# Optimization experiments

Measured on AMD Instinct MI355X. Metric: run time of the kernel, lower is better.

## Reference

```python
import jax, jax.numpy as jnp
import numpy as np

B = 2            # batch size
GRID = 256       # BEV grid H = W
M = 30000        # number of pillars (voxels)
NPTS = 200000    # number of points
IN_C = 16
VOXEL = 0.4      # voxel_size[:2]
PC_MIN = -51.2   # pc_range[:2]
DS = 2           # prod(ds_layer_strides)


def _bn(x, g, b):
    # eval-mode BatchNorm with running_mean=0, running_var=1 (eps absorbed into g)
    return x * g + b


def _conv(x, k, stride):
    # 3x3 conv, padding=1 (spconv SparseConv2d / SubMConv2d with pad k//2), NHWC
    return jax.lax.conv_general_dilated(
        x, k, (stride, stride), ((1, 1), (1, 1)),
        dimension_numbers=('NHWC', 'HWIO', 'NHWC'))


def _active_mask(occ, stride):
    # active output sites of a sparse conv = any active input in the 3x3 receptive field
    pooled = jax.lax.reduce_window(occ, -jnp.inf, jax.lax.max,
                                   (1, 3, 3, 1), (1, stride, stride, 1),
                                   ((0, 0), (1, 1), (1, 1), (0, 0)))
    return (pooled > 0).astype(occ.dtype)


def _forward(features, pfn_w0, pfn_g0, pfn_b0, pfn_w1, pfn_g1, pfn_b1,
             b1_kd, b1_gd, b1_bd, b1_k1, b1_g1, b1_b1, b1_k2, b1_g2, b1_b2,
             b2_kd, b2_gd, b2_bd, b2_k1, b2_g1, b2_b1, b2_k2, b2_g2, b2_b2,
             unq, unq_inv, grid_size):
    # pillar mode: cols 0:2 are xy; convert to (fractional) voxel coordinates
    pos = (features[:, :2] - PC_MIN) / VOXEL  # [N,2] = (px, py)

    # PFN layer 0 (not last): linear(16->16) + BN + ReLU, concat per-pillar max
    h = jax.nn.relu(_bn(features @ pfn_w0, pfn_g0, pfn_b0))            # [N,16]
    hmax = jax.ops.segment_max(h, unq_inv, num_segments=M)             # [M,16]
    h = jnp.concatenate([h, hmax[unq_inv]], axis=1)                    # [N,32]
    # PFN layer 1 (last): linear(32->64) + BN + ReLU
    h = jax.nn.relu(_bn(h @ pfn_w1, pfn_g1, pfn_b1))                   # [N,64]

    # scatter_max pooling points -> pillars
    fv = jax.ops.segment_max(h, unq_inv, num_segments=M)               # [M,64]

    Hn = grid_size
    img = jnp.zeros((B, Hn, Hn, fv.shape[1]), fv.dtype)
    img = img.at[unq[:, 0], unq[:, 1], unq[:, 2]].set(fv)              # dense BEV, NHWC
    occ = jnp.zeros((B, Hn, Hn, 1), fv.dtype)
    occ = occ.at[unq[:, 0], unq[:, 1], unq[:, 2]].set(1.0)

    # block 1: SparseConvBlock(stride=1) + SparseBasicBlock (dense math, masked to active sites)
    occ1 = _active_mask(occ, 1)
    x = jax.nn.relu(_bn(_conv(img, b1_kd, 1), b1_gd, b1_bd)) * occ1
    y = jax.nn.relu(_bn(_conv(x, b1_k1, 1), b1_g1, b1_b1)) * occ1
    y = _bn(_conv(y, b1_k2, 1), b1_g2, b1_b2) * occ1
    x = jax.nn.relu(x + y)

    # block 2: SparseConvBlock(stride=2) + SparseBasicBlock
    occ2 = _active_mask(occ1, 2)
    x = jax.nn.relu(_bn(_conv(x, b2_kd, 2), b2_gd, b2_bd)) * occ2
    y = jax.nn.relu(_bn(_conv(x, b2_k1, 1), b2_g1, b2_b1)) * occ2
    y = _bn(_conv(y, b2_k2, 1), b2_g2, b2_b2) * occ2
    x = jax.nn.relu(x + y)                                             # [B,H/2,W/2,128]

    # bilinear gather at per-point downsampled positions (px -> W axis, py -> H axis)
    bidx = unq[unq_inv, 0]
    px = pos[:, 0] / DS
    py = pos[:, 1] / DS
    Hc, Wc = x.shape[1], x.shape[2]
    x0 = jnp.clip(jnp.floor(px).astype(jnp.int32), 0, Wc - 1)
    x1 = jnp.clip(jnp.floor(px).astype(jnp.int32) + 1, 0, Wc - 1)
    y0 = jnp.clip(jnp.floor(py).astype(jnp.int32), 0, Hc - 1)
    y1 = jnp.clip(jnp.floor(py).astype(jnp.int32) + 1, 0, Hc - 1)
    Ia = x[bidx, y0, x0]
    Ib = x[bidx, y1, x0]
    Ic = x[bidx, y0, x1]
    Id = x[bidx, y1, x1]
    x0f, x1f = x0.astype(px.dtype), x1.astype(px.dtype)
    y0f, y1f = y0.astype(py.dtype), y1.astype(py.dtype)
    wa = ((x1f - px) * (y1f - py))[:, None]
    wb = ((x1f - px) * (py - y0f))[:, None]
    wc = ((px - x0f) * (y1f - py))[:, None]
    wd = ((px - x0f) * (py - y0f))[:, None]
    return Ia * wa + Ib * wb + Ic * wc + Id * wd                       # [N,128]


def setup_inputs() -> dict:
    rng = np.random.default_rng(0)
    d = {}
    d['features'] = jnp.asarray(rng.standard_normal((NPTS, IN_C)).astype(np.float32))
    # unique voxel coords (batch, y, x)
    lin = rng.choice(B * GRID * GRID, size=M, replace=False)
    d['unq'] = jnp.asarray(np.stack([lin // (GRID * GRID), (lin // GRID) % GRID, lin % GRID], 1).astype(np.int32))
    # every pillar gets at least one point
    d['unq_inv'] = jnp.asarray(np.concatenate([np.arange(M), rng.integers(0, M, NPTS - M)]).astype(np.int32))
    d['grid_size'] = GRID

    def w(*s):
        fan = int(np.prod(s[:-1]))
        return jnp.asarray((rng.standard_normal(s) / np.sqrt(fan)).astype(np.float32))

    def g(c):
        return jnp.asarray((0.5 + 0.5 * rng.random(c)).astype(np.float32))

    def bb(c):
        return jnp.asarray((0.1 * rng.standard_normal(c)).astype(np.float32))

    d['pfn_w0'] = w(IN_C, 16); d['pfn_g0'] = g(16); d['pfn_b0'] = bb(16)
    d['pfn_w1'] = w(32, 64);   d['pfn_g1'] = g(64); d['pfn_b1'] = bb(64)
    d['b1_kd'] = w(3, 3, 64, 64);   d['b1_gd'] = g(64);  d['b1_bd'] = bb(64)
    d['b1_k1'] = w(3, 3, 64, 64);   d['b1_g1'] = g(64);  d['b1_b1'] = bb(64)
    d['b1_k2'] = w(3, 3, 64, 64);   d['b1_g2'] = g(64);  d['b1_b2'] = bb(64)
    d['b2_kd'] = w(3, 3, 64, 128);  d['b2_gd'] = g(128); d['b2_bd'] = bb(128)
    d['b2_k1'] = w(3, 3, 128, 128); d['b2_g1'] = g(128); d['b2_b1'] = bb(128)
    d['b2_k2'] = w(3, 3, 128, 128); d['b2_g2'] = g(128); d['b2_b2'] = bb(128)
    return d


def reference(features, unq, unq_inv, grid_size,
              pfn_w0, pfn_g0, pfn_b0, pfn_w1, pfn_g1, pfn_b1,
              b1_kd, b1_gd, b1_bd, b1_k1, b1_g1, b1_b1, b1_k2, b1_g2, b1_b2,
              b2_kd, b2_gd, b2_bd, b2_k1, b2_g1, b2_b1, b2_k2, b2_g2, b2_b2):
    return _forward(features, pfn_w0, pfn_g0, pfn_b0, pfn_w1, pfn_g1, pfn_b1,
                    b1_kd, b1_gd, b1_bd, b1_k1, b1_g1, b1_b1, b1_k2, b1_g2, b1_b2,
                    b2_kd, b2_gd, b2_bd, b2_k1, b2_g1, b2_b1, b2_k2, b2_g2, b2_b2,
                    unq, unq_inv, grid_size)
```

## Files before the change

### kernel.cpp

```cpp
#include <hip/hip_runtime.h>
#include <hip/hip_bf16.h>

#define NPTS    200000
#define MPIL    30000
#define BATCH   2
#define GRID0   256
#define PCMIN   (-51.2f)
#define VOXEL0  (0.4f)
#define NCHUNK  118

#define SLOT_B  ((size_t)16777216)
#define SLOT_F  ((size_t)33554432)

#define W0F 0
#define W1F 256
#define FB1 9216
#define FB2 156672
#define FB3 304128
#define FB4 451584
#define FB5 746496
#define FB6 1336320

#define WS_FLAG 0
#define WS_OCC8 64
#define WS_OCC1 (64 + 131072)
#define WS_OCC2 (64 + 262144)
#define WS_HMAX 393280
#define WS_CNT  2313280
#define WS_OFF  2433280
#define WS_CUR  2553344
#define WS_IDX  2673344
#define WS_LOC  3473344
#define WS_BS   3593344
#define WS_FX   393344

typedef __attribute__((ext_vector_type(8))) short v8s;
typedef __attribute__((ext_vector_type(4))) float f32x4;

static __device__ __forceinline__ float b2f(__hip_bfloat16 v) { return __bfloat162float(v); }
static __device__ __forceinline__ unsigned short f2bbits(float f) {
    __hip_bfloat16 h = __float2bfloat16(f);
    union { __hip_bfloat16 h; unsigned short u; } cv; cv.h = h; return cv.u;
}
static __device__ __forceinline__ float bits2f(unsigned short h) {
    union { unsigned int u; float f; } c; c.u = ((unsigned int)h) << 16; return c.f;
}
static __device__ __forceinline__ float lo2f(unsigned int u) {
    union { unsigned int u; float f; } c; c.u = u << 16; return c.f;
}
static __device__ __forceinline__ float hi2f(unsigned int u) {
    union { unsigned int u; float f; } c; c.u = u & 0xFFFF0000u; return c.f;
}
static __device__ __forceinline__ unsigned int pack2(float a, float b) {
    return (unsigned int)f2bbits(a) | ((unsigned int)f2bbits(b) << 16);
}
static __device__ __forceinline__ void split2(float a, float b, unsigned int& hi, unsigned int& lo) {
    unsigned short ha = f2bbits(a), hb = f2bbits(b);
    hi = (unsigned int)ha | ((unsigned int)hb << 16);
    float ra = a - bits2f(ha);
    float rb = b - bits2f(hb);
    lo = (unsigned int)f2bbits(ra) | ((unsigned int)f2bbits(rb) << 16);
}

static __device__ __forceinline__ float ldf(const void* p, size_t i, int isb) {
    return isb ? b2f(((const __hip_bfloat16*)p)[i]) : ((const float*)p)[i];
}
static __device__ __forceinline__ float4 ld4(const void* p, size_t i, int isb) {
    if (isb) {
        uint2 r = *(const uint2*)((const __hip_bfloat16*)p + i);
        return make_float4(lo2f(r.x), hi2f(r.x), lo2f(r.y), hi2f(r.y));
    }
    return *(const float4*)((const float*)p + i);
}
static __device__ __forceinline__ void st4(void* p, size_t i, int isb, float4 v) {
    if (isb) {
        uint2 pk; pk.x = pack2(v.x, v.y); pk.y = pack2(v.z, v.w);
        *(uint2*)((__hip_bfloat16*)p + i) = pk;
    } else {
        *(float4*)((float*)p + i) = v;
    }
}
static __device__ __forceinline__ void* actptr(void* ob, int slot, int isb) {
    return (char*)ob + (size_t)slot * (isb ? SLOT_B : SLOT_F);
}
static __device__ __forceinline__ float* wpool(void* ob, int isb) {
    return (float*)((char*)ob + 3 * (isb ? SLOT_B : SLOT_F));
}

__global__ void probe_kernel(const unsigned short* __restrict__ g0, int* __restrict__ flag) {
    if (threadIdx.x == 0 && blockIdx.x == 0) {
        int ok = 1;
        for (int i = 0; i < 8; i++) {
            unsigned short u = g0[i];
            if (u < 0x3E00 || u >= 0x4000) ok = 0;
        }
        *flag = ok;
    }
}

__global__ __launch_bounds__(256) void cvt_kernel(const void* __restrict__ src, void* ob,
                                                  int woff, int n, const int* __restrict__ flag) {
    int isb = *flag;
    int i = blockIdx.x * 256 + threadIdx.x;
    if (i < n) wpool(ob, isb)[woff + i] = ldf(src, i, isb);
}

__global__ __launch_bounds__(256) void wfrag_kernel(const void* __restrict__ src, void* ob,
                                                    int fb_bytes, int CIN, int COUT,
                                                    const int* __restrict__ flag)
{
    const int isb = *flag;
    const int cnt = 9 * CIN * COUT;
    int e = blockIdx.x * 256 + threadIdx.x;
    if (e >= cnt) return;
    int i = e & 7;
    int l = (e >> 3) & 63;
    int f = e >> 9;
    int nbn = COUT >> 4, kcn = CIN >> 5;
    int nb = f % nbn;
    int kc = (f / nbn) % kcn;
    int tap = f / (nbn * kcn);
    int ci = kc * 32 + (l >> 4) * 8 + i;
    int co = nb * 16 + (l & 15);
    float wv = ldf(src, (size_t)(tap * CIN + ci) * COUT + co, isb);
    unsigned short h = f2bbits(wv);
    float rem = wv - bits2f(h);
    short* wh = (short*)((char*)ob + 3 * (isb ? SLOT_B : SLOT_F) + fb_bytes);
    wh[e] = (short)h;
    wh[cnt + e] = (short)f2bbits(rem);
}

__global__ __launch_bounds__(256) void hist_kernel(const int* __restrict__ unq_inv,
                                                   int* __restrict__ cnt)
{
    int n = blockIdx.x * 256 + threadIdx.x;
    if (n < NPTS) atomicAdd(&cnt[unq_inv[n]], 1);
}

__global__ __launch_bounds__(256) void scan1_kernel(const int* __restrict__ cnt,
                                                    int* __restrict__ loc,
                                                    int* __restrict__ bs)
{
    __shared__ int s[256];
    const int tid = threadIdx.x;
    const int i = blockIdx.x * 256 + tid;
    int v = (i < MPIL) ? cnt[i] : 0;
    s[tid] = v;
    __syncthreads();
#pragma unroll
    for (int d = 1; d < 256; d <<= 1) {
        int t = (tid >= d) ? s[tid - d] : 0;
        __syncthreads();
        s[tid] += t;
        __syncthreads();
    }
    if (i < MPIL) loc[i] = s[tid] - v;
    if (tid == 255) bs[blockIdx.x] = s[255];
}

__global__ __launch_bounds__(128) void scan2_kernel(int* __restrict__ bs)
{
    __shared__ int s[NCHUNK];
    const int tid = threadIdx.x;
    for (int i = tid; i < NCHUNK; i += 128) s[i] = bs[i];
    __syncthreads();
    if (tid == 0) {
        int acc = 0;
        for (int i = 0; i < NCHUNK; i++) { int t = s[i]; s[i] = acc; acc += t; }
    }
    __syncthreads();
    for (int i = tid; i < NCHUNK; i += 128) bs[i] = s[i];
}

__global__ __launch_bounds__(256) void scan3_kernel(const int* __restrict__ loc,
                                                    const int* __restrict__ bs,
                                                    int* __restrict__ off,
                                                    int* __restrict__ cur)
{
    int i = blockIdx.x * 256 + threadIdx.x;
    if (i < MPIL) {
        int e = loc[i] + bs[blockIdx.x];
        off[i] = e; cur[i] = e;
    }
    if (i == 0) off[MPIL] = NPTS;
}

__global__ __launch_bounds__(256) void fill_kernel(const int* __restrict__ unq_inv,
                                                   int* __restrict__ cur,
                                                   int* __restrict__ idxarr)
{
    int n = blockIdx.x * 256 + threadIdx.x;
    if (n >= NPTS) return;
    int p = unq_inv[n];
    int s = atomicAdd(&cur[p], 1);
    idxarr[s] = n;
}

__global__ __launch_bounds__(256) void pfn0_kernel(
    const void* __restrict__ feat, void* ob, const void* __restrict__ g0,
    const void* __restrict__ b0, const int* __restrict__ flag)
{
    const int isb = *flag;
    int n = blockIdx.x * 256 + threadIdx.x;
    if (n >= NPTS) return;
    const float* w0f = wpool(ob, isb) + W0F;
    void* h0 = actptr(ob, 1, isb);
    float f[16];
#pragma unroll
    for (int i = 0; i < 16; i += 4) {
        float4 v = ld4(feat, (size_t)n * 16 + i, isb);
        f[i] = v.x; f[i + 1] = v.y; f[i + 2] = v.z; f[i + 3] = v.w;
    }
#pragma unroll
    for (int co = 0; co < 16; co += 4) {
        float a0 = 0.f, a1 = 0.f, a2 = 0.f, a3 = 0.f;
#pragma unroll
        for (int ci = 0; ci < 16; ci++) {
            float4 w = *(const float4*)&w0f[ci * 16 + co];
            a0 += f[ci] * w.x; a1 += f[ci] * w.y; a2 += f[ci] * w.z; a3 += f[ci] * w.w;
        }
        float o[4] = { a0, a1, a2, a3 };
#pragma unroll
        for (int k = 0; k < 4; k++) {
            float z = o[k] * ldf(g0, co + k, isb) + ldf(b0, co + k, isb);
            o[k] = fmaxf(z, 0.f);
        }
        st4(h0, (size_t)n * 16 + co, isb, make_float4(o[0], o[1], o[2], o[3]));
    }
}

__global__ __launch_bounds__(256) void hmax_kernel(
    void* ob, const int* __restrict__ off, const int* __restrict__ idxarr,
    float* __restrict__ hmax, const int* __restrict__ flag)
{
    const int isb = *flag;
    int t = blockIdx.x * 256 + threadIdx.x;
    if (t >= MPIL * 16) return;
    int p = t >> 4, ch = t & 15;
    const void* h0 = actptr(ob, 1, isb);
    float m = 0.f;
    int s1 = off[p + 1];
    for (int s = off[p]; s < s1; s++) {
        int n = idxarr[s];
        m = fmaxf(m, ldf(h0, (size_t)n * 16 + ch, isb));
    }
    hmax[t] = m;
}

template<bool BF>
static __device__ __forceinline__ void pfn1p_body(
    void* ob, const float* __restrict__ hmax, const void* __restrict__ g1,
    const void* __restrict__ b1, const int* __restrict__ off,
    const int* __restrict__ idxarr, const int* __restrict__ unq,
    unsigned char* __restrict__ occ)
{
    const int lane = threadIdx.x & 63;
    const int p = (blockIdx.x << 2) + (threadIdx.x >> 6);
    if (p >= MPIL) return;
    const int isb = BF ? 1 : 0;
    const float* w1f = wpool(ob, isb) + W1F;
    const void* h0 = actptr(ob, 1, isb);
    void* img = actptr(ob, 0, isb);

    float wcol[32];
#pragma unroll
    for (int k = 0; k < 32; k++) wcol[k] = w1f[k * 64 + lane];
    float base = 0.f;
#pragma unroll
    for (int k = 0; k < 16; k++) base += hmax[(size_t)p * 16 + k] * wcol[16 + k];
    const float g = ldf(g1, lane, isb);
    const float be = ldf(b1, lane, isb);

    float m = 0.f;
    const int s1 = off[p + 1];
    for (int s = off[p]; s < s1; s++) {
        const int n = idxarr[s];
        float h[16];
        if (BF) {
            const unsigned short* hp = (const unsigned short*)h0 + (size_t)n * 16;
            uint4 a = *(const uint4*)hp;
            uint4 c = *(const uint4*)(hp + 8);
            h[0] = lo2f(a.x); h[1] = hi2f(a.x); h[2] = lo2f(a.y); h[3] = hi2f(a.y);
            h[4] = lo2f(a.z); h[5] = hi2f(a.z); h[6] = lo2f(a.w); h[7] = hi2f(a.w);
            h[8] = lo2f(c.x); h[9] = hi2f(c.x); h[10] = lo2f(c.y); h[11] = hi2f(c.y);
            h[12] = lo2f(c.z); h[13] = hi2f(c.z); h[14] = lo2f(c.w); h[15] = hi2f(c.w);
        } else {
            const float* fp = (const float*)h0 + (size_t)n * 16;
#pragma unroll
            for (int i = 0; i < 16; i += 4) {
                float4 v = *(const float4*)(fp + i);
                h[i] = v.x; h[i + 1] = v.y; h[i + 2] = v.z; h[i + 3] = v.w;
            }
        }
        float z = base;
#pragma unroll
        for (int k = 0; k < 16; k++) z += h[k] * wcol[k];
        z = fmaxf(z * g + be, 0.f);
        m = fmaxf(m, z);
    }

    const int bb = unq[p * 3 + 0], yy = unq[p * 3 + 1], xx = unq[p * 3 + 2];
    const size_t site = ((size_t)bb * GRID0 + yy) * GRID0 + xx;
    if (BF) ((unsigned short*)img)[site * 64 + lane] = f2bbits(m);
    else    ((float*)img)[site * 64 + lane] = m;
    if (lane == 0) occ[site] = 1;
}

__global__ __launch_bounds__(256) void pfn1p_kernel(
    void* ob, const float* __restrict__ hmax, const void* __restrict__ g1,
    const void* __restrict__ b1, const int* __restrict__ off,
    const int* __restrict__ idxarr, const int* __restrict__ unq,
    unsigned char* __restrict__ occ, const int* __restrict__ flag)
{
    if (*flag) pfn1p_body<true>(ob, hmax, g1, b1, off, idxarr, unq, occ);
    else       pfn1p_body<false>(ob, hmax, g1, b1, off, idxarr, unq, occ);
}

__global__ __launch_bounds__(256) void dilate1_kernel(const unsigned char* __restrict__ occ,
                                                      unsigned char* __restrict__ occ1)
{
    int idx = blockIdx.x * 256 + threadIdx.x;
    if (idx >= BATCH * GRID0 * GRID0) return;
    int b = idx / (GRID0 * GRID0);
    int r = idx % (GRID0 * GRID0);
    int y = r / GRID0, x = r % GRID0;
    unsigned char v = 0;
#pragma unroll
    for (int dy = -1; dy <= 1; dy++) {
        int yy = y + dy; if (yy < 0 || yy >= GRID0) continue;
#pragma unroll
        for (int dx = -1; dx <= 1; dx++) {
            int xx = x + dx; if (xx < 0 || xx >= GRID0) continue;
            v |= occ[((size_t)b * GRID0 + yy) * GRID0 + xx];
        }
    }
    occ1[idx] = v ? 1 : 0;
}

__global__ __launch_bounds__(256) void dilate2_kernel(const unsigned char* __restrict__ occ1,
                                                      unsigned char* __restrict__ occ2)
{
    int idx = blockIdx.x * 256 + threadIdx.x;
    if (idx >= BATCH * 128 * 128) return;
    int b = idx / (128 * 128);
    int r = idx % (128 * 128);
    int y = r / 128, x = r % 128;
    unsigned char v = 0;
#pragma unroll
    for (int dy = -1; dy <= 1; dy++) {
        int yy = 2 * y + dy; if (yy < 0 || yy >= GRID0) continue;
#pragma unroll
        for (int dx = -1; dx <= 1; dx++) {
            int xx = 2 * x + dx; if (xx < 0 || xx >= GRID0) continue;
            v |= occ1[((size_t)b * GRID0 + yy) * GRID0 + xx];
        }
    }
    occ2[idx] = v ? 1 : 0;
}

template<int CIN, int COUT, int STRIDE, int TROWS, bool ADD_RES, bool BF>
static __device__ __forceinline__ void conv_body(
    short* s_a, const void* in, void* outp, const void* res, const short* wh,
    const void* gamma, const void* beta, const unsigned char* mask,
    int HIN, int WIN, int HOUT, int WOUT)
{
    constexpr int Y_EXT = (TROWS - 1) * STRIDE + 3;
    constexpr int X_EXT = 15 * STRIDE + 3;
    constexpr int PSTR = CIN + 8;
    constexpr int TSZ = Y_EXT * X_EXT * PSTR;
    constexpr int NCH8 = CIN / 8;
    constexpr int WPR = 4 / TROWS;
    constexpr int NBW = COUT / 16 / WPR;

    const int tid = threadIdx.x;
    const int b = blockIdx.z;
    const int oy0 = blockIdx.y * TROWS;
    const int ox0 = blockIdx.x * 16;

    for (int i = tid; i < Y_EXT * X_EXT * NCH8; i += 256) {
        int c8 = i % NCH8;
        int r = i / NCH8;
        int xo = r % X_EXT;
        int dy = r / X_EXT;
        int yin = oy0 * STRIDE - 1 + dy;
        int xin = ox0 * STRIDE - 1 + xo;
        bool inb = (yin >= 0 && yin < HIN && xin >= 0 && xin < WIN);
        int si = (dy * X_EXT + xo) * PSTR + c8 * 8;
        size_t gi = (((size_t)b * HIN + yin) * WIN + xin) * (size_t)CIN + c8 * 8;
        if (BF) {
            uint4 v = make_uint4(0u, 0u, 0u, 0u);
            if (inb) v = *(const uint4*)((const unsigned short*)in + gi);
            *(uint4*)&s_a[si] = v;
        } else {
            float4 va = make_float4(0.f, 0.f, 0.f, 0.f);
            float4 vb = make_float4(0.f, 0.f, 0.f, 0.f);
            if (inb) {
                va = *(const float4*)((const float*)in + gi);
                vb = *(const float4*)((const float*)in + gi + 4);
            }
            uint4 hv, lv;
            split2(va.x, va.y, hv.x, lv.x);
            split2(va.z, va.w, hv.y, lv.y);
            split2(vb.x, vb.y, hv.z, lv.z);
            split2(vb.z, vb.w, hv.w, lv.w);
            *(uint4*)&s_a[si] = hv;
            *(uint4*)&s_a[TSZ + si] = lv;
        }
    }
    __syncthreads();

    const int lane = tid & 63;
    const int w = tid >> 6;
    const int row = w / WPR;
    const int nb0 = (w % WPR) * NBW;
    const int l15 = lane & 15;
    const int lhi = lane >> 4;
    const short* wl = wh + 9 * CIN * COUT;

    f32x4 acc[NBW];
#pragma unroll
    for (int nb = 0; nb < NBW; nb++) acc[nb] = (f32x4){0.f, 0.f, 0.f, 0.f};

#pragma unroll 1
    for (int ky = 0; ky < 3; ky++) {
        const int arow = (row * STRIDE + ky) * X_EXT;
#pragma unroll
        for (int kx = 0; kx < 3; kx++) {
            const int abase = (arow + l15 * STRIDE + kx) * PSTR + lhi * 8;
#pragma unroll
            for (int kc = 0; kc < CIN / 32; kc++) {
                const v8s ah = *(const v8s*)&s_a[abase + kc * 32];
                v8s al;
                if (!BF) al = *(const v8s*)&s_a[TSZ + abase + kc * 32];
                const int f0 = ((ky * 3 + kx) * (CIN / 32) + kc) * (COUT / 16) + nb0;
#pragma unroll
                for (int nb = 0; nb < NBW; nb++) {
                    const size_t off = (size_t)(f0 + nb) * 512 + lane * 8;
                    const v8s bh = *(const v8s*)&wh[off];
                    acc[nb] = __builtin_amdgcn_mfma_f32_16x16x32_bf16(ah, bh, acc[nb], 0, 0, 0);
                    if (!BF) {
                        const v8s bl = *(const v8s*)&wl[off];
                        acc[nb] = __builtin_amdgcn_mfma_f32_16x16x32_bf16(ah, bl, acc[nb], 0, 0, 0);
                        acc[nb] = __builtin_amdgcn_mfma_f32_16x16x32_bf16(al, bh, acc[nb], 0, 0, 0);
                    }
                }
            }
        }
    }

    const int oy = oy0 + row;
    const size_t mrow = ((size_t)b * HOUT + oy) * WOUT + ox0 + lhi * 4;
    float mk[4];
#pragma unroll
    for (int r = 0; r < 4; r++) mk[r] = mask[mrow + r] ? 1.f : 0.f;

    __syncthreads();

    if constexpr (BF) {
        unsigned short* sw = (unsigned short*)s_a + (size_t)w * 16 * NBW * 16;
#pragma unroll
        for (int nb = 0; nb < NBW; nb++) {
            const int n = (nb0 + nb) * 16 + l15;
            const float g = ldf(gamma, n, 1);
            const float be = ldf(beta, n, 1);
#pragma unroll
            for (int r = 0; r < 4; r++) {
                const size_t oaddr = (mrow + r) * COUT + n;
                float z = acc[nb][r] * g + be;
                z *= mk[r];
                if constexpr (ADD_RES) z += ldf(res, oaddr, 1);
                z = fmaxf(z, 0.f);
                sw[(lhi * 4 + r) * (NBW * 16) + nb * 16 + l15] = f2bbits(z);
            }
        }
        const size_t rowbase = ((size_t)b * HOUT + oy) * WOUT + ox0;
        constexpr int CHUNKS = NBW * 2;
#pragma unroll
        for (int c = lane; c < 16 * CHUNKS; c += 64) {
            const int px = c / CHUNKS, part = c % CHUNKS;
            uint4 v = *(uint4*)&sw[px * (NBW * 16) + part * 8];
            *(uint4*)((unsigned short*)outp + (rowbase + px) * COUT + nb0 * 16 + part * 8) = v;
        }
    } else {
#pragma unroll
        for (int nb = 0; nb < NBW; nb++) {
            const int n = (nb0 + nb) * 16 + l15;
            const float g = ldf(gamma, n, 0);
            const float be = ldf(beta, n, 0);
#pragma unroll
            for (int r = 0; r < 4; r++) {
                const size_t oaddr = (mrow + r) * COUT + n;
                float z = acc[nb][r] * g + be;
                z *= mk[r];
                if constexpr (ADD_RES) z += ldf(res, oaddr, 0);
                ((float*)outp)[oaddr] = fmaxf(z, 0.f);
            }
        }
    }
}

template<int CIN, int COUT, int STRIDE, int TROWS, bool ADD_RES>
__global__ __launch_bounds__(256) void convmf_kernel(
    void* ob, int in_slot, int out_slot, void* out_ws, int res_slot, int fb_bytes,
    const void* __restrict__ gamma, const void* __restrict__ beta,
    const unsigned char* __restrict__ mask, const int* __restrict__ flag,
    int HIN, int WIN, int HOUT, int WOUT)
{
    constexpr int Y_EXT = (TROWS - 1) * STRIDE + 3;
    constexpr int X_EXT = 15 * STRIDE + 3;
    constexpr int PSTR = CIN + 8;
    constexpr int TSZ = Y_EXT * X_EXT * PSTR;
    __shared__ __align__(16) short s_a[2 * TSZ];

    const int isb = *flag;
    const void* in = actptr(ob, in_slot, isb);
    void* outp = out_ws ? out_ws : actptr(ob, out_slot, isb);
    const void* res = ADD_RES ? actptr(ob, res_slot, isb) : nullptr;
    const short* wh = (const short*)((const char*)ob + 3 * (isb ? SLOT_B : SLOT_F) + fb_bytes);

    if (isb)
        conv_body<CIN, COUT, STRIDE, TROWS, ADD_RES, true>(s_a, in, outp, res, wh,
                                                           gamma, beta, mask, HIN, WIN, HOUT, WOUT);
    else
        conv_body<CIN, COUT, STRIDE, TROWS, ADD_RES, false>(s_a, in, outp, res, wh,
                                                            gamma, beta, mask, HIN, WIN, HOUT, WOUT);
}

__global__ __launch_bounds__(256) void gather_kernel(
    const void* __restrict__ x, const void* __restrict__ feat,
    const int* __restrict__ unq, const int* __restrict__ unq_inv,
    void* __restrict__ out, const int* __restrict__ flag)
{
    const int isb = *flag;
    int idx = blockIdx.x * 256 + threadIdx.x;
    if (idx >= NPTS * 32) return;
    int n = idx >> 5;
    int co = (idx & 31) * 4;
    float fx = ldf(feat, (size_t)n * 16 + 0, isb);
    float fy = ldf(feat, (size_t)n * 16 + 1, isb);
    float px = ((fx - PCMIN) / VOXEL0) / 2.0f;
    float py = ((fy - PCMIN) / VOXEL0) / 2.0f;
    int bi = unq[(size_t)unq_inv[n] * 3 + 0];
    int xf = (int)floorf(px), yf = (int)floorf(py);
    int x0 = min(max(xf, 0), 127), x1 = min(max(xf + 1, 0), 127);
    int y0 = min(max(yf, 0), 127), y1 = min(max(yf + 1, 0), 127);
    float x0f = (float)x0, x1f = (float)x1, y0f = (float)y0, y1f = (float)y1;
    float wa = (x1f - px) * (y1f - py);
    float wb = (x1f - px) * (py - y0f);
    float wc = (px - x0f) * (y1f - py);
    float wd = (px - x0f) * (py - y0f);
    size_t base = (size_t)bi * 128 * 128 * 128;
    float4 Ia = ld4(x, base + ((size_t)y0 * 128 + x0) * 128 + co, isb);
    float4 Ib = ld4(x, base + ((size_t)y1 * 128 + x0) * 128 + co, isb);
    float4 Ic = ld4(x, base + ((size_t)y0 * 128 + x1) * 128 + co, isb);
    float4 Id = ld4(x, base + ((size_t)y1 * 128 + x1) * 128 + co, isb);
    float4 r;
    r.x = Ia.x * wa + Ib.x * wb + Ic.x * wc + Id.x * wd;
    r.y = Ia.y * wa + Ib.y * wb + Ic.y * wc + Id.y * wd;
    r.z = Ia.z * wa + Ib.z * wb + Ic.z * wc + Id.z * wd;
    r.w = Ia.w * wa + Ib.w * wb + Ic.w * wc + Id.w * wd;
    st4(out, (size_t)n * 128 + co, isb, r);
}

extern "C" void kernel_launch(void* const* d_in, const int* in_sizes, int n_in,
                              void* d_out, int out_size, void* d_ws, size_t ws_size,
                              hipStream_t stream)
{
    (void)in_sizes; (void)n_in; (void)out_size; (void)ws_size;
    const int* unq = (const int*)d_in[1];
    const int* unq_inv = (const int*)d_in[2];

    char* ws = (char*)d_ws;
    int* flagp = (int*)(ws + WS_FLAG);
    unsigned char* occ8 = (unsigned char*)(ws + WS_OCC8);
    unsigned char* occ1m = (unsigned char*)(ws + WS_OCC1);
    unsigned char* occ2m = (unsigned char*)(ws + WS_OCC2);
    float* hmax = (float*)(ws + WS_HMAX);
    int* cnt = (int*)(ws + WS_CNT);
    int* off = (int*)(ws + WS_OFF);
    int* cur = (int*)(ws + WS_CUR);
    int* idxarr = (int*)(ws + WS_IDX);
    int* loc = (int*)(ws + WS_LOC);
    int* bs = (int*)(ws + WS_BS);
    void* Fx = (void*)(ws + WS_FX);

    probe_kernel<<<1, 64, 0, stream>>>((const unsigned short*)d_in[5], flagp);

    cvt_kernel<<<1, 256, 0, stream>>>(d_in[4], d_out, W0F, 256, flagp);
    cvt_kernel<<<8, 256, 0, stream>>>(d_in[7], d_out, W1F, 2048, flagp);
    wfrag_kernel<<<144, 256, 0, stream>>>(d_in[10], d_out, FB1, 64, 64, flagp);
    wfrag_kernel<<<144, 256, 0, stream>>>(d_in[13], d_out, FB2, 64, 64, flagp);
    wfrag_kernel<<<144, 256, 0, stream>>>(d_in[16], d_out, FB3, 64, 64, flagp);
    wfrag_kernel<<<288, 256, 0, stream>>>(d_in[19], d_out, FB4, 64, 128, flagp);
    wfrag_kernel<<<576, 256, 0, stream>>>(d_in[22], d_out, FB5, 128, 128, flagp);
    wfrag_kernel<<<576, 256, 0, stream>>>(d_in[25], d_out, FB6, 128, 128, flagp);

    hipMemsetAsync(d_out, 0, SLOT_F, stream);
    hipMemsetAsync(cnt, 0, (size_t)MPIL * 4, stream);
    hipMemsetAsync(occ8, 0, 131072, stream);

    hist_kernel<<<(NPTS + 255) / 256, 256, 0, stream>>>(unq_inv, cnt);
    scan1_kernel<<<NCHUNK, 256, 0, stream>>>(cnt, loc, bs);
    scan2_kernel<<<1, 128, 0, stream>>>(bs);
    scan3_kernel<<<NCHUNK, 256, 0, stream>>>(loc, bs, off, cur);
    fill_kernel<<<(NPTS + 255) / 256, 256, 0, stream>>>(unq_inv, cur, idxarr);
    pfn0_kernel<<<(NPTS + 255) / 256, 256, 0, stream>>>(d_in[0], d_out, d_in[5], d_in[6], flagp);
    hmax_kernel<<<(MPIL * 16 + 255) / 256, 256, 0, stream>>>(d_out, off, idxarr, hmax, flagp);
    pfn1p_kernel<<<(MPIL + 3) / 4, 256, 0, stream>>>(d_out, hmax, d_in[8], d_in[9],
                                                     off, idxarr, unq, occ8, flagp);

    dilate1_kernel<<<(BATCH * GRID0 * GRID0) / 256, 256, 0, stream>>>(occ8, occ1m);
    dilate2_kernel<<<(BATCH * 128 * 128) / 256, 256, 0, stream>>>(occ1m, occ2m);

    dim3 blk(256);
    dim3 g1(16, 64, BATCH);
    convmf_kernel<64, 64, 1, 4, false><<<g1, blk, 0, stream>>>(
        d_out, 0, 1, nullptr, 0, FB1, d_in[11], d_in[12], occ1m, flagp, 256, 256, 256, 256);
    convmf_kernel<64, 64, 1, 4, false><<<g1, blk, 0, stream>>>(
        d_out, 1, 2, nullptr, 0, FB2, d_in[14], d_in[15], occ1m, flagp, 256, 256, 256, 256);
    convmf_kernel<64, 64, 1, 4, true><<<g1, blk, 0, stream>>>(
        d_out, 2, 0, nullptr, 1, FB3, d_in[17], d_in[18], occ1m, flagp, 256, 256, 256, 256);
    dim3 g2a(8, 64, BATCH), g2b(8, 64, BATCH);
    convmf_kernel<64, 128, 2, 2, false><<<g2a, blk, 0, stream>>>(
        d_out, 0, 1, nullptr, 0, FB4, d_in[20], d_in[21], occ2m, flagp, 256, 256, 128, 128);
    convmf_kernel<128, 128, 1, 2, false><<<g2b, blk, 0, stream>>>(
        d_out, 1, 2, nullptr, 0, FB5, d_in[23], d_in[24], occ2m, flagp, 128, 128, 128, 128);
    convmf_kernel<128, 128, 1, 2, true><<<g2b, blk, 0, stream>>>(
        d_out, 2, 0, Fx, 1, FB6, d_in[26], d_in[27], occ2m, flagp, 128, 128, 128, 128);

    gather_kernel<<<(NPTS * 32) / 256, 256, 0, stream>>>(Fx, d_in[0], unq, unq_inv,
                                                         d_out, flagp);
}
```

Baseline: 575.8 us.

## Remap conv workgroups across XCDs and prefetch mask/residual before MFMA loop

```diff
diff --git a/kernel.cpp b/kernel.cpp
--- a/kernel.cpp
+++ b/kernel.cpp
@@ -362,7 +362,7 @@
 static __device__ __forceinline__ void conv_body(
     short* s_a, const void* in, void* outp, const void* res, const short* wh,
     const void* gamma, const void* beta, const unsigned char* mask,
-    int HIN, int WIN, int HOUT, int WOUT)
+    int HIN, int WIN, int HOUT, int WOUT, int bx, int by, int bz)
 {
     constexpr int Y_EXT = (TROWS - 1) * STRIDE + 3;
     constexpr int X_EXT = 15 * STRIDE + 3;
@@ -373,9 +373,9 @@
     constexpr int NBW = COUT / 16 / WPR;
 
     const int tid = threadIdx.x;
-    const int b = blockIdx.z;
-    const int oy0 = blockIdx.y * TROWS;
-    const int ox0 = blockIdx.x * 16;
+    const int b = bz;
+    const int oy0 = by * TROWS;
+    const int ox0 = bx * 16;
 
     for (int i = tid; i < Y_EXT * X_EXT * NCH8; i += 256) {
         int c8 = i % NCH8;
@@ -407,7 +407,6 @@
             *(uint4*)&s_a[TSZ + si] = lv;
         }
     }
-    __syncthreads();
 
     const int lane = tid & 63;
     const int w = tid >> 6;
@@ -416,6 +415,24 @@
     const int l15 = lane & 15;
     const int lhi = lane >> 4;
     const short* wl = wh + 9 * CIN * COUT;
+
+    const int oy = oy0 + row;
+    const size_t mrow = ((size_t)b * HOUT + oy) * WOUT + ox0 + lhi * 4;
+    float mk[4];
+#pragma unroll
+    for (int r = 0; r < 4; r++) mk[r] = mask[mrow + r] ? 1.f : 0.f;
+    float rv[NBW][4];
+    if constexpr (ADD_RES) {
+#pragma unroll
+        for (int nb = 0; nb < NBW; nb++) {
+            const int n = (nb0 + nb) * 16 + l15;
+#pragma unroll
+            for (int r = 0; r < 4; r++)
+                rv[nb][r] = ldf(res, (mrow + r) * COUT + n, BF ? 1 : 0);
+        }
+    }
+
+    __syncthreads();
 
     f32x4 acc[NBW];
 #pragma unroll
@@ -448,15 +465,8 @@
         }
     }
 
-    const int oy = oy0 + row;
-    const size_t mrow = ((size_t)b * HOUT + oy) * WOUT + ox0 + lhi * 4;
-    float mk[4];
-#pragma unroll
-    for (int r = 0; r < 4; r++) mk[r] = mask[mrow + r] ? 1.f : 0.f;
-
-    __syncthreads();
-
     if constexpr (BF) {
+        __syncthreads();
         unsigned short* sw = (unsigned short*)s_a + (size_t)w * 16 * NBW * 16;
 #pragma unroll
         for (int nb = 0; nb < NBW; nb++) {
@@ -465,10 +475,9 @@
             const float be = ldf(beta, n, 1);
 #pragma unroll
             for (int r = 0; r < 4; r++) {
-                const size_t oaddr = (mrow + r) * COUT + n;
                 float z = acc[nb][r] * g + be;
                 z *= mk[r];
-                if constexpr (ADD_RES) z += ldf(res, oaddr, 1);
+                if constexpr (ADD_RES) z += rv[nb][r];
                 z = fmaxf(z, 0.f);
                 sw[(lhi * 4 + r) * (NBW * 16) + nb * 16 + l15] = f2bbits(z);
             }
@@ -492,7 +501,7 @@
                 const size_t oaddr = (mrow + r) * COUT + n;
                 float z = acc[nb][r] * g + be;
                 z *= mk[r];
-                if constexpr (ADD_RES) z += ldf(res, oaddr, 0);
+                if constexpr (ADD_RES) z += rv[nb][r];
                 ((float*)outp)[oaddr] = fmaxf(z, 0.f);
             }
         }
@@ -512,6 +521,14 @@
     constexpr int TSZ = Y_EXT * X_EXT * PSTR;
     __shared__ __align__(16) short s_a[2 * TSZ];
 
+    const int nbx = gridDim.x, nby = gridDim.y;
+    const int nwg = nbx * nby * (int)gridDim.z;
+    int bid = blockIdx.x + nbx * (blockIdx.y + nby * blockIdx.z);
+    bid = (bid & 7) * (nwg >> 3) + (bid >> 3);
+    const int bx = bid % nbx;
+    const int byy = (bid / nbx) % nby;
+    const int bz = bid / (nbx * nby);
+
     const int isb = *flag;
     const void* in = actptr(ob, in_slot, isb);
     void* outp = out_ws ? out_ws : actptr(ob, out_slot, isb);
@@ -520,10 +537,12 @@
 
     if (isb)
         conv_body<CIN, COUT, STRIDE, TROWS, ADD_RES, true>(s_a, in, outp, res, wh,
-                                                           gamma, beta, mask, HIN, WIN, HOUT, WOUT);
+                                                           gamma, beta, mask, HIN, WIN, HOUT, WOUT,
+                                                           bx, byy, bz);
     else
         conv_body<CIN, COUT, STRIDE, TROWS, ADD_RES, false>(s_a, in, outp, res, wh,
-                                                            gamma, beta, mask, HIN, WIN, HOUT, WOUT);
+                                                            gamma, beta, mask, HIN, WIN, HOUT, WOUT,
+                                                            bx, byy, bz);
 }
 
 __global__ __launch_bounds__(256) void gather_kernel(
```

Result: no change. 566.7 us (-1.6%).
